# Kernel tuning notes

Hardware: AMD Instinct MI355X
Metric: run time of the kernel (lower is better)

The kernel has to match this reference:

```python
import jax, jax.numpy as jnp
import numpy as np
from jax import lax

PATCH_SIZE = 7


def _census_weight(patch_size, dtype=jnp.float32):
    oc = patch_size * patch_size
    w = np.eye(oc).reshape((patch_size, patch_size, 1, oc))
    w = np.transpose(w, (3, 2, 0, 1))  # [oc, 1, p, p] (OIHW)
    return jnp.asarray(w, dtype=dtype)


def _transform(t, w, patch_size):
    # t: [B, C, H, W] -> grayscale [B, 1, H, W]
    g = t.mean(axis=1, keepdims=True)
    pad = patch_size // 2
    # identity conv gathers the p*p neighborhood into channels: [B, p*p, H, W]
    patches = lax.conv_general_dilated(
        g, w.astype(g.dtype), window_strides=(1, 1),
        padding=[(pad, pad), (pad, pad)],
        dimension_numbers=('NCHW', 'OIHW', 'NCHW'))
    loc_diff = patches - g
    return loc_diff / jnp.sqrt(0.81 + loc_diff ** 2)


def _valid_mask(x, patch_size):
    pad = patch_size // 2
    b, _, h, w = x.shape
    inner = jnp.ones((b, 1, h - 2 * pad, w - 2 * pad), dtype=x.dtype)
    return jnp.pad(inner, ((0, 0), (0, 0), (pad, pad), (pad, pad)))


def setup_inputs() -> dict:
    key = jax.random.key(0)
    k1, k2 = jax.random.split(key)
    x = jax.random.uniform(k1, (8, 3, 256, 256), dtype=jnp.float32)
    y = jax.random.uniform(k2, (8, 3, 256, 256), dtype=jnp.float32)
    return {"x": x, "y": y}


def reference(x, y):
    w = _census_weight(PATCH_SIZE, x.dtype)
    ld_x = _transform(x, w, PATCH_SIZE)
    ld_y = _transform(y, w, PATCH_SIZE)
    diff = ld_x - lax.stop_gradient(ld_y)  # matches .detach()
    dist = (diff ** 2 / (0.1 + diff ** 2)).mean(axis=1, keepdims=True)
    mask = _valid_mask(x, PATCH_SIZE)
    return (dist * mask).mean()
```

## Files before the change

### kernel.cpp

```cpp
#include <hip/hip_runtime.h>

#define HW      256
#define TILE    32
#define HALO    3
#define PSIDE   (TILE + 2*HALO)
#define LSTRIDE (PSIDE + 2)

__global__ __launch_bounds__(256) void census_loss_kernel(
    const float* __restrict__ x, const float* __restrict__ y,
    float* __restrict__ out)
{
    __shared__ float sgx[PSIDE][LSTRIDE];
    __shared__ float sgy[PSIDE][LSTRIDE];

    const int b   = blockIdx.z;
    const int ti0 = blockIdx.y * TILE;
    const int tj0 = blockIdx.x * TILE;

    const float* xb = x + (size_t)b * 3 * HW * HW;
    const float* yb = y + (size_t)b * 3 * HW * HW;

    const int tid = threadIdx.x;
    const float third = 1.0f / 3.0f;

    for (int li = tid; li < PSIDE * PSIDE; li += 256) {
        int r = li / PSIDE;
        int c = li - r * PSIDE;
        int gi = ti0 + r - HALO;
        int gj = tj0 + c - HALO;
        float gx = 0.0f, gy = 0.0f;
        if ((unsigned)gi < HW && (unsigned)gj < HW) {
            int o = gi * HW + gj;
            gx = (xb[o] + xb[o + HW*HW] + xb[o + 2*HW*HW]) * third;
            gy = (yb[o] + yb[o + HW*HW] + yb[o + 2*HW*HW]) * third;
        }
        sgx[r][c] = gx;
        sgy[r][c] = gy;
    }
    __syncthreads();

    const int tx  = tid & 31;
    const int tyb = tid >> 5;
    float acc = 0.0f;

    #pragma unroll
    for (int k = 0; k < 4; ++k) {
        const int ly = tyb + 8 * k;
        const int gi = ti0 + ly;
        const int gj = tj0 + tx;
        if (gi >= HALO && gi < HW - HALO && gj >= HALO && gj < HW - HALO) {
            const float cx = sgx[ly + HALO][tx + HALO];
            const float cy = sgy[ly + HALO][tx + HALO];
            #pragma unroll
            for (int dy = 0; dy < 7; ++dy) {
                #pragma unroll
                for (int dx = 0; dx < 7; ++dx) {
                    float nx = sgx[ly + dy][tx + dx];
                    float ny = sgy[ly + dy][tx + dx];
                    float ux = nx - cx;
                    float uy = ny - cy;
                    float fx = ux * __builtin_amdgcn_rsqf(0.81f + ux * ux);
                    float fy = uy * __builtin_amdgcn_rsqf(0.81f + uy * uy);
                    float d  = fx - fy;
                    float d2 = d * d;
                    acc += d2 * __builtin_amdgcn_rcpf(0.1f + d2);
                }
            }
        }
    }

    #pragma unroll
    for (int off = 32; off > 0; off >>= 1)
        acc += __shfl_down(acc, off, 64);

    __shared__ float wsum[4];
    const int lane = tid & 63;
    const int wid  = tid >> 6;
    if (lane == 0) wsum[wid] = acc;
    __syncthreads();
    if (tid == 0) {
        float s = wsum[0] + wsum[1] + wsum[2] + wsum[3];
        const float scale = 1.0f / (49.0f * 8.0f * 256.0f * 256.0f);
        atomicAdd(out, s * scale);
    }
}

extern "C" void kernel_launch(void* const* d_in, const int* in_sizes, int n_in,
                              void* d_out, int out_size, void* d_ws, size_t ws_size,
                              hipStream_t stream) {
    const float* x = (const float*)d_in[0];
    const float* y = (const float*)d_in[1];
    float* out = (float*)d_out;

    hipMemsetAsync(out, 0, sizeof(float) * out_size, stream);

    dim3 grid(HW / TILE, HW / TILE, 8);
    dim3 block(256);
    census_loss_kernel<<<grid, block, 0, stream>>>(x, y, out);
}
```

Before: 80.52 us.

## Use 32x16 tiles with two vertically adjacent pixels per thread sharing row loads

New measurement: 81.17 us. About the same (+0.8%).

```diff
diff --git a/kernel.cpp b/kernel.cpp
--- a/kernel.cpp
+++ b/kernel.cpp
@@ -1,21 +1,23 @@
 #include <hip/hip_runtime.h>
 
-#define HW      256
-#define TILE    32
-#define HALO    3
-#define PSIDE   (TILE + 2*HALO)
-#define LSTRIDE (PSIDE + 2)
+#define HW    256
+#define TW    32
+#define TH    16
+#define HALO  3
+#define PROWS (TH + 2*HALO)
+#define PCOLS (TW + 2*HALO)
+#define LSTRIDE (PCOLS + 2)
 
 __global__ __launch_bounds__(256) void census_loss_kernel(
     const float* __restrict__ x, const float* __restrict__ y,
     float* __restrict__ out)
 {
-    __shared__ float sgx[PSIDE][LSTRIDE];
-    __shared__ float sgy[PSIDE][LSTRIDE];
+    __shared__ float sgx[PROWS][LSTRIDE];
+    __shared__ float sgy[PROWS][LSTRIDE];
 
     const int b   = blockIdx.z;
-    const int ti0 = blockIdx.y * TILE;
-    const int tj0 = blockIdx.x * TILE;
+    const int ti0 = blockIdx.y * TH;
+    const int tj0 = blockIdx.x * TW;
 
     const float* xb = x + (size_t)b * 3 * HW * HW;
     const float* yb = y + (size_t)b * 3 * HW * HW;
@@ -23,9 +25,9 @@
     const int tid = threadIdx.x;
     const float third = 1.0f / 3.0f;
 
-    for (int li = tid; li < PSIDE * PSIDE; li += 256) {
-        int r = li / PSIDE;
-        int c = li - r * PSIDE;
+    for (int li = tid; li < PROWS * PCOLS; li += 256) {
+        int r = li / PCOLS;
+        int c = li - r * PCOLS;
         int gi = ti0 + r - HALO;
         int gj = tj0 + c - HALO;
         float gx = 0.0f, gy = 0.0f;
@@ -39,35 +41,54 @@
     }
     __syncthreads();
 
-    const int tx  = tid & 31;
-    const int tyb = tid >> 5;
-    float acc = 0.0f;
+    const int tx = tid & 31;
+    const int ty = tid >> 5;
+    const int lr0 = 2 * ty;
+    const int gi0 = ti0 + lr0;
+    const int gj  = tj0 + tx;
+
+    const float cx0 = sgx[lr0 + 3][tx + 3];
+    const float cy0 = sgy[lr0 + 3][tx + 3];
+    const float cx1 = sgx[lr0 + 4][tx + 3];
+    const float cy1 = sgy[lr0 + 4][tx + 3];
+
+    float acc0 = 0.0f, acc1 = 0.0f;
 
     #pragma unroll
-    for (int k = 0; k < 4; ++k) {
-        const int ly = tyb + 8 * k;
-        const int gi = ti0 + ly;
-        const int gj = tj0 + tx;
-        if (gi >= HALO && gi < HW - HALO && gj >= HALO && gj < HW - HALO) {
-            const float cx = sgx[ly + HALO][tx + HALO];
-            const float cy = sgy[ly + HALO][tx + HALO];
-            #pragma unroll
-            for (int dy = 0; dy < 7; ++dy) {
-                #pragma unroll
-                for (int dx = 0; dx < 7; ++dx) {
-                    float nx = sgx[ly + dy][tx + dx];
-                    float ny = sgy[ly + dy][tx + dx];
-                    float ux = nx - cx;
-                    float uy = ny - cy;
-                    float fx = ux * __builtin_amdgcn_rsqf(0.81f + ux * ux);
-                    float fy = uy * __builtin_amdgcn_rsqf(0.81f + uy * uy);
-                    float d  = fx - fy;
-                    float d2 = d * d;
-                    acc += d2 * __builtin_amdgcn_rcpf(0.1f + d2);
-                }
+    for (int r = 0; r < 8; ++r) {
+        float nx[7], ny[7];
+        #pragma unroll
+        for (int dx = 0; dx < 7; ++dx) {
+            nx[dx] = sgx[lr0 + r][tx + dx];
+            ny[dx] = sgy[lr0 + r][tx + dx];
+        }
+        #pragma unroll
+        for (int dx = 0; dx < 7; ++dx) {
+            if (r <= 6) {
+                float ux = nx[dx] - cx0;
+                float uy = ny[dx] - cy0;
+                float fx = ux * __builtin_amdgcn_rsqf(0.81f + ux * ux);
+                float fy = uy * __builtin_amdgcn_rsqf(0.81f + uy * uy);
+                float d  = fx - fy;
+                float d2 = d * d;
+                acc0 += d2 * __builtin_amdgcn_rcpf(0.1f + d2);
+            }
+            if (r >= 1) {
+                float ux = nx[dx] - cx1;
+                float uy = ny[dx] - cy1;
+                float fx = ux * __builtin_amdgcn_rsqf(0.81f + ux * ux);
+                float fy = uy * __builtin_amdgcn_rsqf(0.81f + uy * uy);
+                float d  = fx - fy;
+                float d2 = d * d;
+                acc1 += d2 * __builtin_amdgcn_rcpf(0.1f + d2);
             }
         }
     }
+
+    const bool colv = (gj >= HALO) && (gj < HW - HALO);
+    const bool v0 = colv && (gi0     >= HALO) && (gi0     < HW - HALO);
+    const bool v1 = colv && (gi0 + 1 >= HALO) && (gi0 + 1 < HW - HALO);
+    float acc = (v0 ? acc0 : 0.0f) + (v1 ? acc1 : 0.0f);
 
     #pragma unroll
     for (int off = 32; off > 0; off >>= 1)
@@ -94,7 +115,7 @@
 
     hipMemsetAsync(out, 0, sizeof(float) * out_size, stream);
 
-    dim3 grid(HW / TILE, HW / TILE, 8);
+    dim3 grid(HW / TW, HW / TH, 8);
     dim3 block(256);
     census_loss_kernel<<<grid, block, 0, stream>>>(x, y, out);
 }
```
